# Kernel optimization log

Hardware: AMD Instinct MI355X
Metric: run time of the kernel (lower is better)

Reference implementation:

```python
import jax, jax.numpy as jnp
import numpy as np

HEAD_K_DIM = 128  # linear_key_head_dim (not derivable from weight shapes alone)
EPS_NORM = 1e-6


def _l2norm(x, eps=1e-6):
    return x * jax.lax.rsqrt(jnp.sum(x * x, axis=-1, keepdims=True) + eps)


def setup_inputs() -> dict:
    key = jax.random.key(0)
    ks = jax.random.split(key, 9)
    B, S, H = 2, 1024, 2048
    Hv, Hk, Dk, Dv, K = 32, 16, 128, 128, 4
    key_dim, value_dim = Hk * Dk, Hv * Dv
    C = 2 * key_dim + value_dim  # conv_dim = 8192
    s = 0.02
    return {
        "hidden_states": jax.random.normal(ks[0], (B, S, H), jnp.float32),
        "conv_state": jnp.zeros((B, C, K - 1), jnp.float32),
        "recurrent_state": jnp.zeros((B, Hv, Dk, Dv), jnp.float32),
        "W_qkv": (jax.random.normal(ks[1], (C, H)) * s).astype(jnp.float32),
        "W_z": (jax.random.normal(ks[2], (value_dim, H)) * s).astype(jnp.float32),
        "W_b": (jax.random.normal(ks[3], (Hv, H)) * s).astype(jnp.float32),
        "W_a": (jax.random.normal(ks[4], (Hv, H)) * s).astype(jnp.float32),
        "conv_w": (jax.random.normal(ks[5], (C, K)) * s).astype(jnp.float32),
        "dt_bias": jnp.ones((Hv,), jnp.float32),
        "A_log": jnp.log(jax.random.uniform(ks[6], (Hv,), jnp.float32, 1e-3, 16.0)),
        "norm_weight": jnp.ones((Dv,), jnp.float32),
        "W_out": (jax.random.normal(ks[7], (H, value_dim)) * s).astype(jnp.float32),
    }


def reference(hidden_states, conv_state, recurrent_state, W_qkv, W_z, W_b, W_a,
              conv_w, dt_bias, A_log, norm_weight, W_out):
    B, S, H = hidden_states.shape
    Hv = dt_bias.shape[0]
    Dv = norm_weight.shape[0]
    C, K = conv_w.shape
    value_dim = Hv * Dv
    key_dim = (C - value_dim) // 2
    Dk = HEAD_K_DIM
    Hk = key_dim // Dk

    # input projections
    mixed_qkv = jnp.einsum('bsh,ch->bcs', hidden_states, W_qkv)  # (B, C, S)
    z = hidden_states @ W_z.T                                    # (B, S, value_dim)
    b = hidden_states @ W_b.T                                    # (B, S, Hv)
    a = hidden_states @ W_a.T                                    # (B, S, Hv)

    # causal depthwise conv over time with cached prefix state
    padded = jnp.concatenate([conv_state, mixed_qkv], axis=-1)   # (B, C, K-1+S)
    conv_out = sum(padded[:, :, k:k + S] * conv_w[:, k][None, :, None]
                   for k in range(K))                            # (B, C, S)
    conv_state_new = padded[:, :, -(K - 1):]
    mixed = jnp.swapaxes(jax.nn.silu(conv_out), 1, 2)            # (B, S, C)

    q = mixed[..., :key_dim].reshape(B, S, Hk, Dk)
    k = mixed[..., key_dim:2 * key_dim].reshape(B, S, Hk, Dk)
    v = mixed[..., 2 * key_dim:].reshape(B, S, Hv, Dv)

    beta = jax.nn.sigmoid(b)                                     # (B, S, Hv)
    g = -jnp.exp(A_log) * jax.nn.softplus(a + dt_bias)           # (B, S, Hv)

    rep = Hv // Hk
    if rep > 1:
        q = jnp.repeat(q, rep, axis=2)
        k = jnp.repeat(k, rep, axis=2)

    scale = Dk ** (-0.5)
    q = _l2norm(q) * scale
    k = _l2norm(k)

    # time-leading for scan: (S, B, Hv, ...)
    qT, kT, vT = (jnp.moveaxis(x, 1, 0) for x in (q, k, v))
    gT, betaT = jnp.moveaxis(g, 1, 0), jnp.moveaxis(beta, 1, 0)

    def step(state, xs):
        q_t, k_t, v_t, g_t, beta_t = xs
        state = state * jnp.exp(g_t)[..., None, None]            # decay
        kv_mem = jnp.einsum('bhk,bhkv->bhv', k_t, state)         # read
        delta = (v_t - kv_mem) * beta_t[..., None]               # correction
        state = state + jnp.einsum('bhk,bhv->bhkv', k_t, delta)  # write
        out_t = jnp.einsum('bhk,bhkv->bhv', q_t, state)          # readout
        return state, out_t

    final_state, outs = jax.lax.scan(step, recurrent_state.astype(jnp.float32),
                                     (qT, kT, vT, gT, betaT))
    core = jnp.moveaxis(outs, 0, 1)                              # (B, S, Hv, Dv)

    # gated RMS norm per value head
    var = jnp.mean(core * core, axis=-1, keepdims=True)
    xn = core * jax.lax.rsqrt(var + EPS_NORM) * norm_weight
    gated = xn * jax.nn.silu(z.reshape(B, S, Hv, Dv))

    output = gated.reshape(B, S, value_dim) @ W_out.T            # (B, S, H)
    return output, conv_state_new, final_state
```

## Files before the change

kernel.cpp:

```cpp
#include <hip/hip_runtime.h>
#include <cstdint>
#include <cstddef>

#define B_ 2
#define S_ 1024
#define H_ 2048
#define HV_ 32
#define HK_ 16
#define DK_ 128
#define DV_ 128
#define CC_ 8192
#define KEYDIM_ 2048
#define VALDIM_ 4096
#define NC_ 16
#define CS_ 64
#define NBIG 12416
#define NBIGP 12544

typedef __attribute__((ext_vector_type(8))) short bf16x8;
typedef __attribute__((ext_vector_type(4))) float f32x4;

__device__ __forceinline__ ushort f2bf_rne(float x) {
  union { float f; uint32_t u; } c; c.f = x;
  uint32_t u = c.u + 0x7FFFu + ((c.u >> 16) & 1u);
  return (ushort)(u >> 16);
}

__device__ __forceinline__ void gld16(const void* g, void* l) {
  __builtin_amdgcn_global_load_lds(
      (const __attribute__((address_space(1))) void*)g,
      (__attribute__((address_space(3))) void*)l, 16, 0, 0);
}

__global__ void f2bf_kernel(const float* __restrict__ in, ushort* __restrict__ out, int n) {
  int i = (blockIdx.x * 256 + threadIdx.x) * 4;
  if (i >= n) return;
  float4 v = *(const float4*)(in + i);
  ushort4 o;
  o.x = f2bf_rne(v.x); o.y = f2bf_rne(v.y);
  o.z = f2bf_rne(v.z); o.w = f2bf_rne(v.w);
  *(ushort4*)(out + i) = o;
}

__global__ void wcat_kernel(const float* __restrict__ Wqkv, const float* __restrict__ Wz,
                            const float* __restrict__ Wb, const float* __restrict__ Wa,
                            ushort* __restrict__ out) {
  int i = (blockIdx.x * 256 + threadIdx.x) * 4;
  if (i >= NBIGP * H_) return;
  int n = i >> 11;
  int k = i & (H_ - 1);
  float4 v = make_float4(0.f, 0.f, 0.f, 0.f);
  if (n < 8192)       v = *(const float4*)(Wqkv + (size_t)n * H_ + k);
  else if (n < 12288) v = *(const float4*)(Wz + (size_t)(n - 8192) * H_ + k);
  else if (n < 12320) v = *(const float4*)(Wb + (size_t)(n - 12288) * H_ + k);
  else if (n < 12352) v = *(const float4*)(Wa + (size_t)(n - 12320) * H_ + k);
  ushort4 o;
  o.x = f2bf_rne(v.x); o.y = f2bf_rne(v.y);
  o.z = f2bf_rne(v.z); o.w = f2bf_rne(v.w);
  *(ushort4*)(out + i) = o;
}

#define MEMF() asm volatile("" ::: "memory")
#define VMW(n) asm volatile("s_waitcnt vmcnt(" #n ")" ::: "memory")
#define LGKM(n) asm volatile("s_waitcnt lgkmcnt(" #n ")" ::: "memory")
#define BARR() do { __builtin_amdgcn_s_barrier(); MEMF(); } while (0)

__global__ __launch_bounds__(512, 2) void gemm256_8ph(
    const ushort* __restrict__ A, const ushort* __restrict__ B,
    float* __restrict__ C, int Ns, int K)
{
  __shared__ ushort sAm[2][16384];
  __shared__ ushort sBm[2][16384];

  const int t = threadIdx.x;
  const int wave = t >> 6, lane = t & 63;
  const int wm = wave >> 2, wn = wave & 3;
  const int l15 = lane & 15, l4 = lane >> 4;
  const int mt = blockIdx.x, nt = blockIdx.y;

  const int rgS0 = (wave & 3) + (wave >> 2) * 8;
  const int rgS3 = rgS0 + 4;
  const int rgS1 = (wave & 1) + (wave >> 1) * 4;
  const int rgS2 = rgS1 + 2;

  const ushort* aP0 = A + (size_t)(mt * 256 + rgS0 * 16 + l15) * K + l4 * 8;
  const ushort* aP1 = A + (size_t)(mt * 256 + rgS3 * 16 + l15) * K + l4 * 8;
  const ushort* bP0 = B + (size_t)(nt * 256 + rgS1 * 16 + l15) * K + l4 * 8;
  const ushort* bP1 = B + (size_t)(nt * 256 + rgS2 * 16 + l15) * K + l4 * 8;

  f32x4 acc[8][4];
  #pragma unroll
  for (int i = 0; i < 8; i++)
    #pragma unroll
    for (int j = 0; j < 4; j++)
      #pragma unroll
      for (int r = 0; r < 4; r++) acc[i][j][r] = 0.f;

  bf16x8 aF[8], bF[4];

  gld16(aP0,      &sAm[0][(rgS0 * 2 + 0) * 512]);
  gld16(aP1,      &sAm[0][(rgS3 * 2 + 0) * 512]);
  gld16(bP0,      &sBm[0][(rgS1 * 2 + 0) * 512]);
  gld16(bP1,      &sBm[0][(rgS2 * 2 + 0) * 512]);
  MEMF();
  gld16(aP0 + 32, &sAm[0][(rgS0 * 2 + 1) * 512]);
  gld16(aP1 + 32, &sAm[0][(rgS3 * 2 + 1) * 512]);
  gld16(bP0 + 32, &sBm[0][(rgS1 * 2 + 1) * 512]);
  gld16(bP1 + 32, &sBm[0][(rgS2 * 2 + 1) * 512]);
  MEMF();
  VMW(4); BARR();

  const int NT = K >> 6;
  for (int tt = 0; tt < NT; tt++) {
    const int c = tt & 1, o = c ^ 1;
    const int kq = (tt + 1 < NT) ? (tt + 1) << 6 : 0;
    #pragma unroll
    for (int h = 0; h < 2; h++) {
      #pragma unroll
      for (int i = 0; i < 8; i++)
        aF[i] = *(const bf16x8*)(&sAm[c][((wm * 8 + i) * 2 + h) * 512 + lane * 8]);
      #pragma unroll
      for (int j = 0; j < 4; j++)
        bF[j] = *(const bf16x8*)(&sBm[c][((wn * 4 + j) * 2 + h) * 512 + lane * 8]);
      MEMF();
      gld16(aP0 + kq + h * 32, &sAm[o][(rgS0 * 2 + h) * 512]);
      gld16(aP1 + kq + h * 32, &sAm[o][(rgS3 * 2 + h) * 512]);
      gld16(bP0 + kq + h * 32, &sBm[o][(rgS1 * 2 + h) * 512]);
      gld16(bP1 + kq + h * 32, &sBm[o][(rgS2 * 2 + h) * 512]);
      MEMF();
      LGKM(8);
      BARR();
      LGKM(0);
      __builtin_amdgcn_sched_barrier(0);
      __builtin_amdgcn_s_setprio(1);
      #pragma unroll
      for (int i = 0; i < 8; i++)
        #pragma unroll
        for (int j = 0; j < 4; j++)
          acc[i][j] = __builtin_amdgcn_mfma_f32_16x16x32_bf16(aF[i], bF[j], acc[i][j], 0, 0, 0);
      __builtin_amdgcn_s_setprio(0);
      VMW(4);
      BARR();
    }
  }
  VMW(0);

  #pragma unroll
  for (int mf = 0; mf < 8; mf++) {
    const int row0 = mt * 256 + wm * 128 + mf * 16 + l4 * 4;
    #pragma unroll
    for (int nf = 0; nf < 4; nf++) {
      const int col = nt * 256 + wn * 64 + nf * 16 + l15;
      if (col < Ns) {
        #pragma unroll
        for (int r = 0; r < 4; r++)
          C[(size_t)(row0 + r) * Ns + col] = acc[mf][nf][r];
      }
    }
  }
}

__device__ __forceinline__ void stage_tile(
    const ushort* aS0, const ushort* aS1, const ushort* bS0, const ushort* bS1,
    ushort* ldsA, ushort* ldsB, int wave, int k0)
{
  #pragma unroll
  for (int h = 0; h < 2; h++) {
    gld16(aS0 + k0 + h * 32, ldsA + h * 4096 + (wave * 2 + 0) * 512);
    gld16(aS1 + k0 + h * 32, ldsA + h * 4096 + (wave * 2 + 1) * 512);
    gld16(bS0 + k0 + h * 32, ldsB + h * 4096 + (wave * 2 + 0) * 512);
    gld16(bS1 + k0 + h * 32, ldsB + h * 4096 + (wave * 2 + 1) * 512);
  }
}

__global__ __launch_bounds__(256) void gemm_bf16_nt(
    const ushort* __restrict__ A, const ushort* __restrict__ B,
    float* __restrict__ C, int M, int N, int K)
{
  __shared__ ushort sL[2][2][8192];
  int t = threadIdx.x;
  int wave = t >> 6, lane = t & 63;
  int wm = wave >> 1, wn = wave & 1;
  int lrow = lane & 15, quad = lane >> 4;
  int mt = blockIdx.x, nt = blockIdx.y;

  f32x4 acc[4][4];
  #pragma unroll
  for (int i = 0; i < 4; i++)
    #pragma unroll
    for (int j = 0; j < 4; j++)
      #pragma unroll
      for (int r = 0; r < 4; r++) acc[i][j][r] = 0.f;

  const ushort* aS0 = A + (size_t)(mt * 128 + (wave * 2 + 0) * 16 + lrow) * K + quad * 8;
  const ushort* aS1 = A + (size_t)(mt * 128 + (wave * 2 + 1) * 16 + lrow) * K + quad * 8;
  const ushort* bS0 = B + (size_t)(nt * 128 + (wave * 2 + 0) * 16 + lrow) * K + quad * 8;
  const ushort* bS1 = B + (size_t)(nt * 128 + (wave * 2 + 1) * 16 + lrow) * K + quad * 8;

  stage_tile(aS0, aS1, bS0, bS1, &sL[0][0][0], &sL[0][1][0], wave, 0);
  __syncthreads();

  const int NK = K >> 6;
  for (int it = 0; it < NK; it++) {
    if (it + 1 < NK)
      stage_tile(aS0, aS1, bS0, bS1,
                 &sL[(it + 1) & 1][0][0], &sL[(it + 1) & 1][1][0],
                 wave, (it + 1) * 64);
    const ushort* bufA = &sL[it & 1][0][0];
    const ushort* bufB = &sL[it & 1][1][0];
    #pragma unroll
    for (int h = 0; h < 2; h++) {
      bf16x8 af[4], bfr[4];
      #pragma unroll
      for (int i = 0; i < 4; i++)
        af[i] = *(const bf16x8*)(bufA + h * 4096 + (wm * 4 + i) * 512 + lane * 8);
      #pragma unroll
      for (int j = 0; j < 4; j++)
        bfr[j] = *(const bf16x8*)(bufB + h * 4096 + (wn * 4 + j) * 512 + lane * 8);
      #pragma unroll
      for (int i = 0; i < 4; i++)
        #pragma unroll
        for (int j = 0; j < 4; j++)
          acc[i][j] = __builtin_amdgcn_mfma_f32_16x16x32_bf16(af[i], bfr[j], acc[i][j], 0, 0, 0);
    }
    __syncthreads();
  }

  #pragma unroll
  for (int i = 0; i < 4; i++) {
    int m_base = mt * 128 + wm * 64 + i * 16 + quad * 4;
    #pragma unroll
    for (int j = 0; j < 4; j++) {
      int n = nt * 128 + wn * 64 + j * 16 + lrow;
      #pragma unroll
      for (int rr = 0; rr < 4; rr++)
        C[(size_t)(m_base + rr) * N + n] = acc[i][j][rr];
    }
  }
}

__global__ void convstate_kernel(const float* __restrict__ Cbig,
                                 float* __restrict__ out)
{
  int idx = blockIdx.x * blockDim.x + threadIdx.x;
  if (idx >= B_ * CC_ * 3) return;
  int j = idx % 3;
  int c = (idx / 3) % CC_;
  int b = idx / (3 * CC_);
  out[idx] = Cbig[((size_t)(b * S_ + (S_ - 3 + j))) * NBIG + c];
}

__global__ __launch_bounds__(128) void prep_qkv(
    const float* __restrict__ Cbig, const float* __restrict__ conv_state,
    const float* __restrict__ conv_w,
    float* __restrict__ Qn, float* __restrict__ Kn, float* __restrict__ Vb)
{
  int group = blockIdx.x, s = blockIdx.y, b = blockIdx.z;
  int t = threadIdx.x;
  int c = group * 128 + t;
  float acc = 0.f;
  #pragma unroll
  for (int kk = 0; kk < 4; kk++) {
    int sp = s - 3 + kk;
    float x = (sp < 0) ? conv_state[((size_t)(b * CC_ + c)) * 3 + (3 + sp)]
                       : Cbig[((size_t)(b * S_ + sp)) * NBIG + c];
    acc += conv_w[c * 4 + kk] * x;
  }
  float val = acc / (1.f + __expf(-acc));

  if (group < 32) {
    __shared__ float red2[2];
    float p = val * val;
    #pragma unroll
    for (int off = 32; off > 0; off >>= 1) p += __shfl_xor(p, off);
    if ((t & 63) == 0) red2[t >> 6] = p;
    __syncthreads();
    float r = rsqrtf(red2[0] + red2[1] + 1e-6f);
    if (group < 16) {
      r *= 0.08838834764831845f;
      Qn[(((size_t)(b * HK_ + group)) * S_ + s) * DK_ + t] = val * r;
    } else {
      Kn[(((size_t)(b * HK_ + (group - 16))) * S_ + s) * DK_ + t] = val * r;
    }
  } else {
    Vb[(((size_t)(b * HV_ + (group - 32))) * S_ + s) * DV_ + t] = val;
  }
}

__global__ void prep_gb(const float* __restrict__ Cbig,
                        const float* __restrict__ A_log, const float* __restrict__ dt_bias,
                        float* __restrict__ g_buf, float* __restrict__ beta_buf)
{
  int idx = blockIdx.x * blockDim.x + threadIdx.x;
  if (idx >= B_ * HV_ * S_) return;
  int s = idx & (S_ - 1);
  int hv = (idx >> 10) & 31;
  int b = idx >> 15;
  float bv = Cbig[((size_t)(b * S_ + s)) * NBIG + 12288 + hv];
  float av = Cbig[((size_t)(b * S_ + s)) * NBIG + 12320 + hv];
  float x = av + dt_bias[hv];
  float sp = (x > 20.f) ? x : log1pf(__expf(x));
  g_buf[idx] = -__expf(A_log[hv]) * sp;
  beta_buf[idx] = 1.f / (1.f + __expf(-bv));
}

__device__ __forceinline__ int swf4(int r, int f) { return r * 32 + (f ^ (r & 31)); }

__global__ __launch_bounds__(256) void cp_kernel(
    const float* __restrict__ Qn, const float* __restrict__ Kn,
    const float* __restrict__ Vb,
    const float* __restrict__ g_buf, const float* __restrict__ beta_buf,
    float* __restrict__ G_buf, float* __restrict__ M_buf,
    float* __restrict__ KcD, float* __restrict__ D0p)
{
  __shared__ float sK[64 * 128];
  __shared__ float sX[32 * 128];
  __shared__ float sT[64 * 65];
  __shared__ float sGB[128];
  float* sG  = sGB;
  float* sBe = sGB + 64;
  float* sA  = sX;
  float* tTw = sX;
  float* tTb = sX;
  float4* sK4 = (float4*)sK;
  float4* sX4 = (float4*)sX;

  const int ch = blockIdx.x;
  const int bh = ch / NC_, c = ch % NC_;
  const int b = bh >> 5, hv = bh & 31, hk = hv >> 1;
  const int s0 = c * CS_;
  const int t = threadIdx.x;
  const size_t gOff = (size_t)bh * S_ + s0;

  if (t < 64) {
    float Gw0 = g_buf[gOff + t];
    #pragma unroll
    for (int off = 1; off < 64; off <<= 1) {
      float o = __shfl_up(Gw0, off);
      if (t >= off) Gw0 += o;
    }
    G_buf[gOff + t] = Gw0;
    sG[t] = Gw0;
    sBe[t] = beta_buf[gOff + t];
  }
  {
    const float4* src = (const float4*)(Kn + ((size_t)(b * HK_ + hk) * S_ + s0) * DK_);
    #pragma unroll
    for (int u = 0; u < 8; u++) {
      int idx = u * 256 + t;
      sK4[swf4(idx >> 5, idx & 31)] = src[idx];
    }
  }
  __syncthreads();

  const float4* qsrc = (const float4*)(Qn + ((size_t)(b * HK_ + hk) * S_ + s0) * DK_);
  {
    int ti2 = t >> 4, tj = t & 15;
    for (int h = 0; h < 2; h++) {
      #pragma unroll
      for (int u = 0; u < 4; u++) {
        int idx = u * 256 + t;
        sX4[swf4(idx >> 5, idx & 31)] = qsrc[h * 1024 + idx];
      }
      __syncthreads();
      float accM[2][4];
      #pragma unroll
      for (int a = 0; a < 2; a++)
        #pragma unroll
        for (int e = 0; e < 4; e++) accM[a][e] = 0.f;
      for (int k4 = 0; k4 < 32; k4++) {
        float4 qv[2], kv[4];
        qv[0] = sX4[swf4(ti2, k4)];
        qv[1] = sX4[swf4(ti2 + 16, k4)];
        #pragma unroll
        for (int e = 0; e < 4; e++) kv[e] = sK4[swf4(tj + 16 * e, k4)];
        #pragma unroll
        for (int a = 0; a < 2; a++)
          #pragma unroll
          for (int e = 0; e < 4; e++)
            accM[a][e] += qv[a].x * kv[e].x + qv[a].y * kv[e].y +
                          qv[a].z * kv[e].z + qv[a].w * kv[e].w;
      }
      #pragma unroll
      for (int a = 0; a < 2; a++) {
        int iG = h * 32 + ti2 + 16 * a;
        float Gi = sG[iG];
        #pragma unroll
        for (int e = 0; e < 4; e++) {
          int j = tj + 16 * e;
          float m = (j <= iG) ? __expf(Gi - sG[j]) * accM[a][e] : 0.f;
          M_buf[(size_t)ch * 4096 + iG * 64 + j] = m;
        }
      }
      __syncthreads();
    }
  }

  {
    int ti = t >> 4, tj = t & 15;
    float accA[4][4];
    #pragma unroll
    for (int a = 0; a < 4; a++)
      #pragma unroll
      for (int e = 0; e < 4; e++) accA[a][e] = 0.f;
    for (int k4 = 0; k4 < 32; k4++) {
      float4 ki[4], kj[4];
      #pragma unroll
      for (int e = 0; e < 4; e++) {
        ki[e] = sK4[swf4(ti + 16 * e, k4)];
        kj[e] = sK4[swf4(tj + 16 * e, k4)];
      }
      #pragma unroll
      for (int a = 0; a < 4; a++)
        #pragma unroll
        for (int e = 0; e < 4; e++)
          accA[a][e] += ki[a].x * kj[e].x + ki[a].y * kj[e].y +
                        ki[a].z * kj[e].z + ki[a].w * kj[e].w;
    }
    float resA[4][4];
    #pragma unroll
    for (int a = 0; a < 4; a++) {
      int i = ti + 16 * a;
      float Gi = sG[i], Bi = sBe[i];
      #pragma unroll
      for (int e = 0; e < 4; e++) {
        int j = tj + 16 * e;
        resA[a][e] = (j < i) ? Bi * __expf(Gi - sG[j]) * accA[a][e] : 0.f;
      }
    }
    __syncthreads();
    #pragma unroll
    for (int a = 0; a < 4; a++)
      #pragma unroll
      for (int e = 0; e < 4; e++)
        sA[(ti + 16 * a) * 64 + (tj + 16 * e)] = resA[a][e];
  }
  __syncthreads();

  if (t < 64) {
    sT[t] = (t == 0) ? 1.f : 0.f;
    for (int i = 1; i < 64; i++) {
      float acc = 0.f;
      for (int j = 0; j < i; j++) acc += sA[i * 64 + j] * sT[j * 65 + t];
      sT[i * 65 + t] = ((t == i) ? 1.f : 0.f) - acc;
    }
  }
  __syncthreads();

  #pragma unroll
  for (int u = 0; u < 16; u++) {
    int idx = u * 256 + t;
    int tcol = idx & 63;
    int j = idx >> 6;
    float wj = sBe[j] * __expf(sG[j]);
    tTw[j * 64 + tcol] = sT[tcol * 65 + j] * wj;
  }
  __syncthreads();

  {
    int i04 = t >> 4, tk = t & 15;
    float accK[4][8];
    #pragma unroll
    for (int r = 0; r < 4; r++)
      #pragma unroll
      for (int u = 0; u < 8; u++) accK[r][u] = 0.f;
    for (int j = 0; j < 64; j++) {
      float4 tw = ((float4*)tTw)[j * 16 + i04];
      float4 ka = sK4[swf4(j, tk * 2)];
      float4 kb = sK4[swf4(j, tk * 2 + 1)];
      float tws[4] = {tw.x, tw.y, tw.z, tw.w};
      float kvv[8] = {ka.x, ka.y, ka.z, ka.w, kb.x, kb.y, kb.z, kb.w};
      #pragma unroll
      for (int r = 0; r < 4; r++)
        #pragma unroll
        for (int u = 0; u < 8; u++)
          accK[r][u] += tws[r] * kvv[u];
    }
    size_t base = (size_t)ch * NBIG;
    #pragma unroll
    for (int r = 0; r < 4; r++) {
      *(float4*)(&KcD[base + (size_t)(i04 * 4 + r) * 128 + tk * 8]) =
          make_float4(accK[r][0], accK[r][1], accK[r][2], accK[r][3]);
      *(float4*)(&KcD[base + (size_t)(i04 * 4 + r) * 128 + tk * 8 + 4]) =
          make_float4(accK[r][4], accK[r][5], accK[r][6], accK[r][7]);
    }
  }
  __syncthreads();

  #pragma unroll
  for (int u = 0; u < 16; u++) {
    int idx = u * 256 + t;
    int tcol = idx & 63;
    int j = idx >> 6;
    tTb[j * 64 + tcol] = sT[tcol * 65 + j] * sBe[j];
  }
  {
    const float4* src = (const float4*)(Vb + ((size_t)bh * S_ + s0) * DV_);
    #pragma unroll
    for (int u = 0; u < 8; u++) {
      int idx = u * 256 + t;
      sK4[swf4(idx >> 5, idx & 31)] = src[idx];
    }
  }
  __syncthreads();

  {
    int i04 = t >> 4, tv_ = t & 15;
    float accD[4][8];
    #pragma unroll
    for (int r = 0; r < 4; r++)
      #pragma unroll
      for (int u = 0; u < 8; u++) accD[r][u] = 0.f;
    for (int j = 0; j < 64; j++) {
      float4 tb = ((float4*)tTb)[j * 16 + i04];
      float4 va = sK4[swf4(j, tv_ * 2)];
      float4 vb = sK4[swf4(j, tv_ * 2 + 1)];
      float tbs[4] = {tb.x, tb.y, tb.z, tb.w};
      float vvv[8] = {va.x, va.y, va.z, va.w, vb.x, vb.y, vb.z, vb.w};
      #pragma unroll
      for (int r = 0; r < 4; r++)
        #pragma unroll
        for (int u = 0; u < 8; u++)
          accD[r][u] += tbs[r] * vvv[u];
    }
    size_t base = (size_t)ch * NBIG;
    #pragma unroll
    for (int r = 0; r < 4; r++) {
      *(float4*)(&D0p[base + (size_t)(i04 * 4 + r) * 128 + tv_ * 8]) =
          make_float4(accD[r][0], accD[r][1], accD[r][2], accD[r][3]);
      *(float4*)(&D0p[base + (size_t)(i04 * 4 + r) * 128 + tv_ * 8 + 4]) =
          make_float4(accD[r][4], accD[r][5], accD[r][6], accD[r][7]);
    }
  }
}

__global__ __launch_bounds__(512) void phaseb_kernel(
    const float* __restrict__ rec_state, const float* __restrict__ Qn,
    const float* __restrict__ Kn, const float* __restrict__ G_buf,
    float* __restrict__ KcD, const float* __restrict__ D0p,
    float* __restrict__ Oq_buf, float* __restrict__ final_state)
{
  __shared__ float sS[128 * 32];
  __shared__ float sKT[128 * 64];
  __shared__ float sQT[128 * 64];
  __shared__ float sD[64 * 32];
  __shared__ float sR[2][64 * 32];
  __shared__ float sGf[1024];

  const int blk = blockIdx.x;
  const int bh = (blk & 7) | ((blk >> 5) << 3);
  const int vq = (blk >> 3) & 3;
  const int b = bh >> 5, hv = bh & 31, hk = hv >> 1;
  const int t = threadIdx.x;
  const int vbase = vq * 32;
  const float* gG = G_buf + (size_t)bh * S_;

  #pragma unroll
  for (int u = 0; u < 2; u++) {
    int idx = u * 512 + t;
    int k = idx >> 3;
    int v4 = (idx & 7) * 4;
    *(float4*)(&sS[k * 32 + v4]) =
        *(const float4*)(&rec_state[((size_t)bh * 128 + k) * 128 + vbase + v4]);
  }
  sGf[t] = gG[t];
  sGf[t + 512] = gG[t + 512];
  __syncthreads();

  const int si = t & 63, skq = t >> 6;
  const int kg = t >> 8;
  const int tt = t & 255;
  const int ti = tt >> 3, tv = t & 7;
  const int tp = t >> 3;

  const float* qBase = Qn + ((size_t)(b * HK_ + hk) * S_ + si) * DK_ + skq * 16;
  const float* kBase = Kn + ((size_t)(b * HK_ + hk) * S_ + si) * DK_ + skq * 16;

  float4 rKc[4], rQ[4], rKn[4], rD0[2];
  {
    const size_t ch0 = (size_t)bh * NC_;
    const float* kcRow = KcD + ch0 * NBIG + si * 128 + skq * 16;
    #pragma unroll
    for (int u = 0; u < 4; u++) {
      rKc[u] = *(const float4*)(kcRow + u * 4);
      rQ[u]  = *(const float4*)(qBase + u * 4);
      rKn[u] = *(const float4*)(kBase + u * 4);
    }
    if (kg == 0) {
      #pragma unroll
      for (int r = 0; r < 2; r++)
        rD0[r] = *(const float4*)(&D0p[ch0 * NBIG + (size_t)(ti * 2 + r) * 128 + vbase + tv * 4]);
    }
  }

  for (int c = 0; c < NC_; c++) {
    const size_t ch = (size_t)bh * NC_ + c;
    const int s0 = c * CS_;
    const int cn = (c + 1 < NC_) ? c + 1 : c;
    const size_t chn = (size_t)bh * NC_ + cn;
    const int s0n = cn * CS_;
    const float GC = sGf[s0 + 63];
    const float eGC = __expf(GC);

    {
      float eGi = __expf(sGf[s0 + si]);
      #pragma unroll
      for (int u = 0; u < 4; u++) {
        float4 kc = rKc[u];
        float4 qv = rQ[u];
        int kk = skq * 16 + u * 4;
        sKT[(kk + 0) * 64 + si] = kc.x; sKT[(kk + 1) * 64 + si] = kc.y;
        sKT[(kk + 2) * 64 + si] = kc.z; sKT[(kk + 3) * 64 + si] = kc.w;
        sQT[(kk + 0) * 64 + si] = qv.x * eGi; sQT[(kk + 1) * 64 + si] = qv.y * eGi;
        sQT[(kk + 2) * 64 + si] = qv.z * eGi; sQT[(kk + 3) * 64 + si] = qv.w * eGi;
      }
    }
    __syncthreads();

    {
      const float* kcRow = KcD + chn * NBIG + si * 128 + skq * 16;
      const float* qRow  = qBase + (size_t)s0n * DK_;
      #pragma unroll
      for (int u = 0; u < 4; u++) {
        rKc[u] = *(const float4*)(kcRow + u * 4);
        rQ[u]  = *(const float4*)(qRow + u * 4);
      }
    }

    {
      float accD[2][4], accO[2][4];
      #pragma unroll
      for (int r = 0; r < 2; r++) {
        accO[r][0] = accO[r][1] = accO[r][2] = accO[r][3] = 0.f;
        accD[r][0] = accD[r][1] = accD[r][2] = accD[r][3] = 0.f;
      }
      if (kg == 0) {
        #pragma unroll
        for (int r = 0; r < 2; r++) {
          accD[r][0] = rD0[r].x; accD[r][1] = rD0[r].y;
          accD[r][2] = rD0[r].z; accD[r][3] = rD0[r].w;
        }
      }
      const int k0 = kg << 6;
      #pragma unroll 4
      for (int k = k0; k < k0 + 64; k++) {
        float2 kc = *(const float2*)(&sKT[k * 64 + ti * 2]);
        float2 qb = *(const float2*)(&sQT[k * 64 + ti * 2]);
        float4 sv = *(const float4*)(&sS[k * 32 + tv * 4]);
        accD[0][0] -= kc.x * sv.x; accD[0][1] -= kc.x * sv.y;
        accD[0][2] -= kc.x * sv.z; accD[0][3] -= kc.x * sv.w;
        accD[1][0] -= kc.y * sv.x; accD[1][1] -= kc.y * sv.y;
        accD[1][2] -= kc.y * sv.z; accD[1][3] -= kc.y * sv.w;
        accO[0][0] += qb.x * sv.x; accO[0][1] += qb.x * sv.y;
        accO[0][2] += qb.x * sv.z; accO[0][3] += qb.x * sv.w;
        accO[1][0] += qb.y * sv.x; accO[1][1] += qb.y * sv.y;
        accO[1][2] += qb.y * sv.z; accO[1][3] += qb.y * sv.w;
      }
      if (kg == 1) {
        #pragma unroll
        for (int r = 0; r < 2; r++) {
          int i = ti * 2 + r;
          *(float4*)(&sR[0][i * 32 + tv * 4]) =
              make_float4(accD[r][0], accD[r][1], accD[r][2], accD[r][3]);
          *(float4*)(&sR[1][i * 32 + tv * 4]) =
              make_float4(accO[r][0], accO[r][1], accO[r][2], accO[r][3]);
        }
      }
      __syncthreads();
      if (kg == 0) {
        #pragma unroll
        for (int r = 0; r < 2; r++) {
          int i = ti * 2 + r;
          float4 pD = *(const float4*)(&sR[0][i * 32 + tv * 4]);
          float4 pO = *(const float4*)(&sR[1][i * 32 + tv * 4]);
          float4 dv = make_float4(accD[r][0] + pD.x, accD[r][1] + pD.y,
                                  accD[r][2] + pD.z, accD[r][3] + pD.w);
          float4 ov = make_float4(accO[r][0] + pO.x, accO[r][1] + pO.y,
                                  accO[r][2] + pO.z, accO[r][3] + pO.w);
          *(float4*)(&sD[i * 32 + tv * 4]) = dv;
          *(float4*)(&KcD[ch * NBIG + (size_t)i * 128 + vbase + tv * 4]) = dv;
          *(float4*)(&Oq_buf[ch * 8192 + (size_t)i * 128 + vbase + tv * 4]) = ov;
        }
        #pragma unroll
        for (int r = 0; r < 2; r++)
          rD0[r] = *(const float4*)(&D0p[chn * NBIG + (size_t)(ti * 2 + r) * 128 + vbase + tv * 4]);
      }
    }

    {
      float sc = __expf(GC - sGf[s0 + si]);
      #pragma unroll
      for (int u = 0; u < 4; u++) {
        float4 x = rKn[u];
        x.x *= sc; x.y *= sc; x.z *= sc; x.w *= sc;
        int kgr = skq * 4 + u;
        *(float4*)(&sKT[si * 128 + 4 * (kgr ^ (si & 31))]) = x;
      }
    }
    {
      const float* kRow = kBase + (size_t)s0n * DK_;
      #pragma unroll
      for (int u = 0; u < 4; u++) rKn[u] = *(const float4*)(kRow + u * 4);
    }
    __syncthreads();

    {
      float acc[2][4];
      acc[0][0] = acc[0][1] = acc[0][2] = acc[0][3] = 0.f;
      acc[1][0] = acc[1][1] = acc[1][2] = acc[1][3] = 0.f;
      const int kgr = tp >> 1, kh = (tp & 1) * 2;
      #pragma unroll 4
      for (int i = 0; i < 64; i++) {
        float4 d  = *(const float4*)(&sD[i * 32 + tv * 4]);
        float2 ka = *(const float2*)(&sKT[i * 128 + 4 * (kgr ^ (i & 31)) + kh]);
        acc[0][0] += ka.x * d.x; acc[0][1] += ka.x * d.y;
        acc[0][2] += ka.x * d.z; acc[0][3] += ka.x * d.w;
        acc[1][0] += ka.y * d.x; acc[1][1] += ka.y * d.y;
        acc[1][2] += ka.y * d.z; acc[1][3] += ka.y * d.w;
      }
      #pragma unroll
      for (int r = 0; r < 2; r++) {
        int k = tp * 2 + r;
        float4 s = *(const float4*)(&sS[k * 32 + tv * 4]);
        s.x = s.x * eGC + acc[r][0]; s.y = s.y * eGC + acc[r][1];
        s.z = s.z * eGC + acc[r][2]; s.w = s.w * eGC + acc[r][3];
        *(float4*)(&sS[k * 32 + tv * 4]) = s;
      }
    }
    __syncthreads();
  }

  #pragma unroll
  for (int u = 0; u < 2; u++) {
    int idx = u * 512 + t;
    int k = idx >> 3;
    int v4 = (idx & 7) * 4;
    *(float4*)(&final_state[((size_t)bh * 128 + k) * 128 + vbase + v4]) =
        *(const float4*)(&sS[k * 32 + v4]);
  }
}

__global__ __launch_bounds__(128) void phasec_kernel(
    const float* __restrict__ KcD, const float* __restrict__ Oq_buf,
    const float* __restrict__ M_buf, const float* __restrict__ norm_weight,
    const float* __restrict__ Cbig, ushort* __restrict__ zg_bf)
{
  __shared__ float sM[4096];
  __shared__ float red[2][2];
  int ch = blockIdx.x;
  int bh = ch / NC_, c = ch % NC_;
  int b = bh >> 5, hv = bh & 31;
  int s0 = c * CS_;
  int v = threadIdx.x;

  float Dr[64];
  #pragma unroll
  for (int j = 0; j < 64; j++) Dr[j] = KcD[(size_t)ch * NBIG + j * 128 + v];
  {
    const float4* src = (const float4*)(M_buf + (size_t)ch * 4096);
    #pragma unroll
    for (int u = 0; u < 8; u++) ((float4*)sM)[u * 128 + v] = src[u * 128 + v];
  }
  __syncthreads();
  float nw = norm_weight[v];

  for (int i = 0; i < 64; i++) {
    float o = Oq_buf[(size_t)ch * 8192 + i * 128 + v];
    const float4* mr = (const float4*)(sM + i * 64);
    #pragma unroll
    for (int j4 = 0; j4 < 16; j4++) {
      float4 m = mr[j4];
      o += m.x * Dr[4 * j4] + m.y * Dr[4 * j4 + 1] +
           m.z * Dr[4 * j4 + 2] + m.w * Dr[4 * j4 + 3];
    }
    float p = o * o;
    #pragma unroll
    for (int off = 32; off > 0; off >>= 1) p += __shfl_xor(p, off);
    if ((v & 63) == 0) red[i & 1][v >> 6] = p;
    __syncthreads();
    float var = (red[i & 1][0] + red[i & 1][1]) * (1.f / 128.f);
    float xn = o * rsqrtf(var + 1e-6f) * nw;
    float zv = Cbig[((size_t)(b * S_ + s0 + i)) * NBIG + 8192 + hv * DV_ + v];
    zg_bf[((size_t)(b * S_ + s0 + i)) * VALDIM_ + hv * DV_ + v] =
        f2bf_rne(xn * (zv / (1.f + __expf(-zv))));
  }
}

extern "C" void kernel_launch(void* const* d_in, const int* in_sizes, int n_in,
                              void* d_out, int out_size, void* d_ws, size_t ws_size,
                              hipStream_t stream)
{
  const float* hs          = (const float*)d_in[0];
  const float* conv_state  = (const float*)d_in[1];
  const float* rec_state   = (const float*)d_in[2];
  const float* W_qkv       = (const float*)d_in[3];
  const float* W_z         = (const float*)d_in[4];
  const float* W_b         = (const float*)d_in[5];
  const float* W_a         = (const float*)d_in[6];
  const float* conv_w      = (const float*)d_in[7];
  const float* dt_bias     = (const float*)d_in[8];
  const float* A_log       = (const float*)d_in[9];
  const float* norm_weight = (const float*)d_in[10];
  const float* W_out       = (const float*)d_in[11];

  float* out       = (float*)d_out;
  float* out_conv  = out + (size_t)B_ * S_ * H_;
  float* out_state = out_conv + (size_t)B_ * CC_ * 3;

  float* ws = (float*)d_ws;
  float* Cbig = ws;
  float* KcD  = Cbig;
  float* D0p  = Cbig + (size_t)1024 * NBIG;
  float* g_buf    = ws + 25427968;
  float* beta_buf = ws + 25493504;
  float* G_buf    = ws + 25559040;
  float* Qn       = ws + 25624576;
  float* Kn       = ws + 29818880;
  float* Vb       = ws + 34013184;
  float* M_buf    = ws + 42401792;
  float* Oq_buf   = Vb;

  ushort* Wcat_bf = (ushort*)(ws + 25427968);
  ushort* hs_bf   = (ushort*)(ws + 38273024);
  ushort* zg_bf   = (ushort*)Qn;
  ushort* Wout_bf = (ushort*)Kn;

  const int M = B_ * S_;

  f2bf_kernel<<<(M * H_) / 1024, 256, 0, stream>>>(hs, hs_bf, M * H_);
  wcat_kernel<<<(NBIGP * H_) / 1024, 256, 0, stream>>>(W_qkv, W_z, W_b, W_a, Wcat_bf);
  gemm256_8ph<<<dim3(M / 256, NBIGP / 256), 512, 0, stream>>>(hs_bf, Wcat_bf, Cbig, NBIG, H_);
  convstate_kernel<<<(B_ * CC_ * 3 + 255) / 256, 256, 0, stream>>>(Cbig, out_conv);
  prep_qkv<<<dim3(64, S_, B_), 128, 0, stream>>>(Cbig, conv_state, conv_w, Qn, Kn, Vb);
  prep_gb<<<(B_ * HV_ * S_ + 255) / 256, 256, 0, stream>>>(Cbig, A_log, dt_bias, g_buf, beta_buf);
  cp_kernel<<<B_ * HV_ * NC_, 256, 0, stream>>>(Qn, Kn, Vb, g_buf, beta_buf,
                                                G_buf, M_buf, KcD, D0p);
  phaseb_kernel<<<B_ * HV_ * 4, 512, 0, stream>>>(rec_state, Qn, Kn, G_buf,
                                                  KcD, D0p, Oq_buf, out_state);
  f2bf_kernel<<<(H_ * VALDIM_) / 1024, 256, 0, stream>>>(W_out, Wout_bf, H_ * VALDIM_);
  phasec_kernel<<<B_ * HV_ * NC_, 128, 0, stream>>>(KcD, Oq_buf, M_buf,
                                                    norm_weight, Cbig, zg_bf);
  gemm_bf16_nt<<<dim3(M / 128, H_ / 128), 256, 0, stream>>>(zg_bf, Wout_bf, out, M, H_, VALDIM_);
}
```

Before: 836.7 us.

## Double-buffer MFMA fragments in registers to overlap LDS reads with matmul

```diff
diff --git a/kernel.cpp b/kernel.cpp
--- a/kernel.cpp
+++ b/kernel.cpp
@@ -62,8 +62,34 @@
 
 #define MEMF() asm volatile("" ::: "memory")
 #define VMW(n) asm volatile("s_waitcnt vmcnt(" #n ")" ::: "memory")
-#define LGKM(n) asm volatile("s_waitcnt lgkmcnt(" #n ")" ::: "memory")
 #define BARR() do { __builtin_amdgcn_s_barrier(); MEMF(); } while (0)
+
+#define RDA(dst, cbuf, h) do { _Pragma("unroll")                                     \
+    for (int i_ = 0; i_ < 8; i_++)                                                   \
+      dst[i_] = *(const bf16x8*)(                                                    \
+          &sAm[cbuf][((wm * 8 + i_) * 2 + (h)) * 512 + lane * 8]); } while (0)
+
+#define RDB(dst, cbuf, h) do { _Pragma("unroll")                                     \
+    for (int j_ = 0; j_ < 4; j_++)                                                   \
+      dst[j_] = *(const bf16x8*)(                                                    \
+          &sBm[cbuf][((wn * 4 + j_) * 2 + (h)) * 512 + lane * 8]); } while (0)
+
+#define MMA(aS, bS) do {                                                             \
+    __builtin_amdgcn_s_setprio(1);                                                   \
+    _Pragma("unroll") for (int i_ = 0; i_ < 8; i_++)                                 \
+    _Pragma("unroll") for (int j_ = 0; j_ < 4; j_++)                                 \
+      acc[i_][j_] = __builtin_amdgcn_mfma_f32_16x16x32_bf16(                         \
+          aS[i_], bS[j_], acc[i_][j_], 0, 0, 0);                                     \
+    __builtin_amdgcn_s_setprio(0);                                                   \
+  } while (0)
+
+#define STG(ob, hh, kqv) do {                                                        \
+    gld16(aP0 + (kqv) + (hh) * 32, &sAm[ob][(rgS0 * 2 + (hh)) * 512]);               \
+    gld16(aP1 + (kqv) + (hh) * 32, &sAm[ob][(rgS3 * 2 + (hh)) * 512]);               \
+    gld16(bP0 + (kqv) + (hh) * 32, &sBm[ob][(rgS1 * 2 + (hh)) * 512]);               \
+    gld16(bP1 + (kqv) + (hh) * 32, &sBm[ob][(rgS2 * 2 + (hh)) * 512]);               \
+    MEMF();                                                                          \
+  } while (0)
 
 __global__ __launch_bounds__(512, 2) void gemm256_8ph(
     const ushort* __restrict__ A, const ushort* __restrict__ B,
@@ -96,52 +122,27 @@
       #pragma unroll
       for (int r = 0; r < 4; r++) acc[i][j][r] = 0.f;
 
-  bf16x8 aF[8], bF[4];
-
-  gld16(aP0,      &sAm[0][(rgS0 * 2 + 0) * 512]);
-  gld16(aP1,      &sAm[0][(rgS3 * 2 + 0) * 512]);
-  gld16(bP0,      &sBm[0][(rgS1 * 2 + 0) * 512]);
-  gld16(bP1,      &sBm[0][(rgS2 * 2 + 0) * 512]);
-  MEMF();
-  gld16(aP0 + 32, &sAm[0][(rgS0 * 2 + 1) * 512]);
-  gld16(aP1 + 32, &sAm[0][(rgS3 * 2 + 1) * 512]);
-  gld16(bP0 + 32, &sBm[0][(rgS1 * 2 + 1) * 512]);
-  gld16(bP1 + 32, &sBm[0][(rgS2 * 2 + 1) * 512]);
-  MEMF();
-  VMW(4); BARR();
+  bf16x8 aA[8], bA[4], aB[8], bB[4];
+
+  STG(0, 0, 0);
+  STG(0, 1, 0);
+  STG(1, 0, 64);
+  VMW(8); BARR();
+  RDA(aA, 0, 0); RDB(bA, 0, 0); MEMF();
 
   const int NT = K >> 6;
   for (int tt = 0; tt < NT; tt++) {
     const int c = tt & 1, o = c ^ 1;
-    const int kq = (tt + 1 < NT) ? (tt + 1) << 6 : 0;
-    #pragma unroll
-    for (int h = 0; h < 2; h++) {
-      #pragma unroll
-      for (int i = 0; i < 8; i++)
-        aF[i] = *(const bf16x8*)(&sAm[c][((wm * 8 + i) * 2 + h) * 512 + lane * 8]);
-      #pragma unroll
-      for (int j = 0; j < 4; j++)
-        bF[j] = *(const bf16x8*)(&sBm[c][((wn * 4 + j) * 2 + h) * 512 + lane * 8]);
-      MEMF();
-      gld16(aP0 + kq + h * 32, &sAm[o][(rgS0 * 2 + h) * 512]);
-      gld16(aP1 + kq + h * 32, &sAm[o][(rgS3 * 2 + h) * 512]);
-      gld16(bP0 + kq + h * 32, &sBm[o][(rgS1 * 2 + h) * 512]);
-      gld16(bP1 + kq + h * 32, &sBm[o][(rgS2 * 2 + h) * 512]);
-      MEMF();
-      LGKM(8);
-      BARR();
-      LGKM(0);
-      __builtin_amdgcn_sched_barrier(0);
-      __builtin_amdgcn_s_setprio(1);
-      #pragma unroll
-      for (int i = 0; i < 8; i++)
-        #pragma unroll
-        for (int j = 0; j < 4; j++)
-          acc[i][j] = __builtin_amdgcn_mfma_f32_16x16x32_bf16(aF[i], bF[j], acc[i][j], 0, 0, 0);
-      __builtin_amdgcn_s_setprio(0);
-      VMW(4);
-      BARR();
-    }
+    const int kq1 = (tt + 1 < NT) ? (tt + 1) << 6 : 0;
+    const int kq2 = (tt + 2 < NT) ? (tt + 2) << 6 : 0;
+    VMW(4); BARR();
+    STG(o, 1, kq1);
+    RDA(aB, c, 1); RDB(bB, c, 1); MEMF();
+    MMA(aA, bA);
+    VMW(4); BARR();
+    STG(c, 0, kq2);
+    RDA(aA, o, 0); RDB(bA, o, 0); MEMF();
+    MMA(aB, bB);
   }
   VMW(0);
 
```

After: 897.8 us. 1.07x slower.
